# Performance work log

Measured on AMD Instinct MI355X. Metric: run time of the kernel, lower is better.

The kernel has to match this reference:

```python
import jax, jax.numpy as jnp
import numpy as np
import math

B, N, M, DK, H = 2, 2048, 2048, 512, 512  # input_v == hidden_size == H


def _lin(x, w, b):
    # torch Linear: y = x @ W.T + b, w: [out, in]
    return jnp.einsum('bnd,od->bno', x, w) + b


def setup_inputs() -> dict:
    key = jax.random.key(0)
    ks = jax.random.split(key, 20)
    s = 0.02
    d = {
        'KEY': jax.random.normal(ks[0], (B, N, DK), jnp.float32),
        'VALUE': jax.random.normal(ks[1], (B, N, H), jnp.float32),
        'QUERY': jax.random.normal(ks[2], (B, M, DK), jnp.float32),
        # W MLP: input_k -> hidden -> hidden -> input_k
        'W1_w': jax.random.normal(ks[3], (H, DK), jnp.float32) * s,
        'W1_b': jnp.zeros((H,), jnp.float32),
        'W2_w': jax.random.normal(ks[4], (H, H), jnp.float32) * s,
        'W2_b': jnp.zeros((H,), jnp.float32),
        'W3_w': jax.random.normal(ks[5], (DK, H), jnp.float32) * s,
        'W3_b': jnp.zeros((DK,), jnp.float32),
        # Wv MLP: input_v -> hidden -> hidden -> hidden
        'V1_w': jax.random.normal(ks[6], (H, H), jnp.float32) * s,
        'V1_b': jnp.zeros((H,), jnp.float32),
        'V2_w': jax.random.normal(ks[7], (H, H), jnp.float32) * s,
        'V2_b': jnp.zeros((H,), jnp.float32),
        'V3_w': jax.random.normal(ks[8], (H, H), jnp.float32) * s,
        'V3_b': jnp.zeros((H,), jnp.float32),
        # Wo: hidden -> input_v
        'Wo_w': jax.random.normal(ks[9], (H, H), jnp.float32) * s,
        'Wo_b': jnp.zeros((H,), jnp.float32),
    }
    return d


def reference(KEY, VALUE, QUERY, W1_w, W1_b, W2_w, W2_b, W3_w, W3_b,
              V1_w, V1_b, V2_w, V2_b, V3_w, V3_b, Wo_w, Wo_b):
    def mlp(x, w1, b1, w2, b2, w3, b3):
        h = jax.nn.relu(_lin(x, w1, b1))
        h = jax.nn.relu(_lin(h, w2, b2))
        return _lin(h, w3, b3)

    Wk = mlp(KEY, W1_w, W1_b, W2_w, W2_b, W3_w, W3_b)      # [b,n,dk]
    Wq = mlp(QUERY, W1_w, W1_b, W2_w, W2_b, W3_w, W3_b)    # [b,m,dk]
    Wv = mlp(VALUE, V1_w, V1_b, V2_w, V2_b, V3_w, V3_b)    # [b,n,h]

    KEY_s = KEY * Wk
    QUERY_s = QUERY * Wq
    VALUE_s = VALUE * Wv

    d_wk = KEY_s.shape[-1]
    dist = jnp.einsum('bij,bkj->bik', KEY_s, QUERY_s) / math.sqrt(d_wk)  # [b,n,m]
    weights = jax.nn.softmax(-(dist ** 2) * 0.5, axis=1)  # softmax over keys
    context = jnp.einsum('bik,bij->bkj', weights, VALUE_s)  # [b,m,h]
    # dropout is identity in eval mode
    return _lin(context, Wo_w, Wo_b)  # [b,m,input_v]
```

## Files before the change

### kernel.cpp

```cpp
#include <hip/hip_runtime.h>
#include <math.h>

typedef unsigned short u16;
typedef unsigned int u32;
typedef __attribute__((ext_vector_type(8))) short short8;
typedef __attribute__((ext_vector_type(4))) float f32x4;
typedef __attribute__((ext_vector_type(4))) u16 u16x4;

__device__ __forceinline__ void gload16(const void* g, void* l) {
    __builtin_amdgcn_global_load_lds(
        (__attribute__((address_space(1))) u32*)g,
        (__attribute__((address_space(3))) u32*)l, 16, 0, 0);
}

__device__ __forceinline__ u16 f2bf_rne(float v) {
    u32 u = __builtin_bit_cast(u32, v);
    return (u16)((u + 0x7FFFu + ((u >> 16) & 1u)) >> 16);
}
__device__ __forceinline__ float bf2f(u16 h) {
    u32 u = ((u32)h) << 16;
    return __builtin_bit_cast(float, u);
}
__device__ __forceinline__ void splt(float v, u16& h, u16& l) {
    h = f2bf_rne(v);
    l = f2bf_rne(v - bf2f(h));
}

enum { EP_RELU, EP_MUL };
enum { EP_DIST16, EP_PART };
enum { RM_CHUNK, RM_DIST2D };

template<int EP>
__global__ __launch_bounds__(256)
void mlp_pf(const u16* __restrict__ Ah, const u16* __restrict__ Al,
            const u16* __restrict__ BHkq, const u16* __restrict__ BLkq,
            const u16* __restrict__ BHv, const u16* __restrict__ BLv,
            const float* __restrict__ bias_kq, const float* __restrict__ bias_v,
            const float* __restrict__ Xk, const float* __restrict__ Xq,
            const float* __restrict__ Xv,
            u16* __restrict__ Ch, u16* __restrict__ Cl)
{
    __shared__ u16 LAh[2][128 * 32];
    __shared__ u16 LAl[2][128 * 32];
    __shared__ u16 LBh[2][64 * 32];
    __shared__ u16 LBl[2][64 * 32];

    const int tid = threadIdx.x;
    const int lane = tid & 63;
    const int wave = tid >> 6;
    const int wr = wave >> 1, wc = wave & 1;
    const int fr = lane & 15, kg = lane >> 4;

    const int L = blockIdx.y * 8 + blockIdx.x;
    const int xcd = L & 7;
    const int i = L >> 3;
    const int panel = xcd * 12 + (i >> 3);
    const int m0 = panel * 128, n0 = (i & 7) * 64;
    const int sec = panel >> 5;

    const u16* Bh = (sec == 2) ? BHv : BHkq;
    const u16* Bl = (sec == 2) ? BLv : BLkq;
    const float* bias = (sec == 2) ? bias_v : bias_kq;

    f32x4 acc[4][2];
    #pragma unroll
    for (int a = 0; a < 4; ++a)
        #pragma unroll
        for (int j = 0; j < 2; ++j)
            acc[a][j] = (f32x4){0.f, 0.f, 0.f, 0.f};

    auto STAGE = [&](int buf, int kk) {
        #pragma unroll
        for (int h = 0; h < 2; ++h) {
            int c = h * 256 + tid;
            long so = (long)(m0 + (c >> 2)) * 512 + kk + (c & 3) * 8;
            gload16(Ah + so, &LAh[buf][c * 8]);
        }
        #pragma unroll
        for (int h = 0; h < 2; ++h) {
            int c = h * 256 + tid;
            long so = (long)(m0 + (c >> 2)) * 512 + kk + (c & 3) * 8;
            gload16(Al + so, &LAl[buf][c * 8]);
        }
        {
            int c = tid;
            long so = (long)(n0 + (c >> 2)) * 512 + kk + (c & 3) * 8;
            gload16(Bh + so, &LBh[buf][c * 8]);
            gload16(Bl + so, &LBl[buf][c * 8]);
        }
    };

    auto COMPUTE = [&](int buf) {
        short8 ah[4], al[4], bh[2], bl[2];
        #pragma unroll
        for (int a = 0; a < 4; ++a) {
            int off = (wr * 64 + a * 16 + fr) * 32 + kg * 8;
            ah[a] = *(const short8*)&LAh[buf][off];
            al[a] = *(const short8*)&LAl[buf][off];
        }
        #pragma unroll
        for (int j = 0; j < 2; ++j) {
            int off = (wc * 32 + j * 16 + fr) * 32 + kg * 8;
            bh[j] = *(const short8*)&LBh[buf][off];
            bl[j] = *(const short8*)&LBl[buf][off];
        }
        #pragma unroll
        for (int a = 0; a < 4; ++a)
            #pragma unroll
            for (int j = 0; j < 2; ++j) {
                acc[a][j] = __builtin_amdgcn_mfma_f32_16x16x32_bf16(ah[a], bh[j], acc[a][j], 0, 0, 0);
                acc[a][j] = __builtin_amdgcn_mfma_f32_16x16x32_bf16(ah[a], bl[j], acc[a][j], 0, 0, 0);
                acc[a][j] = __builtin_amdgcn_mfma_f32_16x16x32_bf16(al[a], bh[j], acc[a][j], 0, 0, 0);
            }
    };

    STAGE(0, 0);
    int cur = 0;
    for (int t = 0; t < 15; ++t) {
        STAGE(cur ^ 1, (t + 1) << 5);
        asm volatile("s_waitcnt vmcnt(6)" ::: "memory");
        __builtin_amdgcn_s_barrier();
        COMPUTE(cur);
        __builtin_amdgcn_s_barrier();
        cur ^= 1;
    }
    asm volatile("s_waitcnt vmcnt(0)" ::: "memory");
    __builtin_amdgcn_s_barrier();
    COMPUTE(cur);

    const float* X = (EP == EP_MUL) ? ((sec == 0) ? Xk : (sec == 1) ? Xq : Xv) : nullptr;

    #pragma unroll
    for (int a = 0; a < 4; ++a)
        #pragma unroll
        for (int j = 0; j < 2; ++j)
            #pragma unroll
            for (int r = 0; r < 4; ++r) {
                int row = m0 + wr * 64 + a * 16 + kg * 4 + r;
                int col = n0 + wc * 32 + j * 16 + fr;
                float v = acc[a][j][r] + bias[col];
                if constexpr (EP == EP_RELU) {
                    v = fmaxf(v, 0.f);
                } else {
                    v *= X[(long)(row - (sec << 12)) * 512 + col];
                }
                long o = (long)row * 512 + col;
                u16 h, l; splt(v, h, l);
                Ch[o] = h; Cl[o] = l;
            }
}

template<int EP, int RM>
__global__ __launch_bounds__(256)
void gemm_pf(int K, int nsl, int KS,
             const u16* __restrict__ Ah, const u16* __restrict__ Al, int lda, long sA,
             const u16* __restrict__ Bh, const u16* __restrict__ Bl, int ldb, long sB,
             float* __restrict__ Cf, u16* __restrict__ Ch, u16* __restrict__ Cl,
             int ldc, long sC)
{
    __shared__ u16 LAh[2][128 * 32];
    __shared__ u16 LAl[2][128 * 32];
    __shared__ u16 LBh[2][64 * 32];
    __shared__ u16 LBl[2][64 * 32];

    const int tid = threadIdx.x;
    const int lane = tid & 63;
    const int wave = tid >> 6;
    const int wr = wave >> 1, wc = wave & 1;
    const int fr = lane & 15, kg = lane >> 4;

    int bx, by, bz;
    {
        const int gx = gridDim.x, gy = gridDim.y;
        const int L = (blockIdx.z * gy + blockIdx.y) * gx + blockIdx.x;
        const int xcd = L & 7;
        const int i = L >> 3;
        if constexpr (RM == RM_DIST2D) {
            const int c = i >> 6, pos = i & 63;
            const int chunk = c * 8 + xcd;
            const int mp = (chunk & 3) * 8 + (pos >> 3);
            bx = (chunk >> 2) * 8 + (pos & 7);
            by = mp & 15;
            bz = mp >> 4;
        } else {
            const int P = gy * gridDim.z;
            const int ppx = P >> 3;
            const int xt = i % gx;
            const int panel = xcd * ppx + i / gx;
            bx = xt;
            by = panel % gy;
            bz = panel / gy;
        }
    }

    const int b = bz / nsl;
    const int s = bz - b * nsl;
    const int k0 = s * KS;
    int k1 = k0 + KS; if (k1 > K) k1 = K;
    const int nt = (k1 - k0) >> 5;

    Ah += b * sA; Al += b * sA;
    Bh += b * sB; Bl += b * sB;
    const long cb = (long)bz * sC;

    const int m0 = by * 128, n0 = bx * 64;

    f32x4 acc[4][2];
    #pragma unroll
    for (int a = 0; a < 4; ++a)
        #pragma unroll
        for (int j = 0; j < 2; ++j)
            acc[a][j] = (f32x4){0.f, 0.f, 0.f, 0.f};

    auto STAGE = [&](int buf, int kk) {
        #pragma unroll
        for (int h = 0; h < 2; ++h) {
            int c = h * 256 + tid;
            long so = (long)(m0 + (c >> 2)) * lda + kk + (c & 3) * 8;
            gload16(Ah + so, &LAh[buf][c * 8]);
        }
        #pragma unroll
        for (int h = 0; h < 2; ++h) {
            int c = h * 256 + tid;
            long so = (long)(m0 + (c >> 2)) * lda + kk + (c & 3) * 8;
            gload16(Al + so, &LAl[buf][c * 8]);
        }
        {
            int c = tid;
            long so = (long)(n0 + (c >> 2)) * ldb + kk + (c & 3) * 8;
            gload16(Bh + so, &LBh[buf][c * 8]);
            gload16(Bl + so, &LBl[buf][c * 8]);
        }
    };

    auto COMPUTE = [&](int buf) {
        short8 ah[4], al[4], bh[2], bl[2];
        #pragma unroll
        for (int a = 0; a < 4; ++a) {
            int off = (wr * 64 + a * 16 + fr) * 32 + kg * 8;
            ah[a] = *(const short8*)&LAh[buf][off];
            al[a] = *(const short8*)&LAl[buf][off];
        }
        #pragma unroll
        for (int j = 0; j < 2; ++j) {
            int off = (wc * 32 + j * 16 + fr) * 32 + kg * 8;
            bh[j] = *(const short8*)&LBh[buf][off];
            bl[j] = *(const short8*)&LBl[buf][off];
        }
        #pragma unroll
        for (int a = 0; a < 4; ++a)
            #pragma unroll
            for (int j = 0; j < 2; ++j) {
                acc[a][j] = __builtin_amdgcn_mfma_f32_16x16x32_bf16(ah[a], bh[j], acc[a][j], 0, 0, 0);
                acc[a][j] = __builtin_amdgcn_mfma_f32_16x16x32_bf16(ah[a], bl[j], acc[a][j], 0, 0, 0);
                acc[a][j] = __builtin_amdgcn_mfma_f32_16x16x32_bf16(al[a], bh[j], acc[a][j], 0, 0, 0);
            }
    };

    STAGE(0, k0);
    int cur = 0;
    for (int t = 0; t < nt - 1; ++t) {
        STAGE(cur ^ 1, k0 + ((t + 1) << 5));
        asm volatile("s_waitcnt vmcnt(6)" ::: "memory");
        __builtin_amdgcn_s_barrier();
        COMPUTE(cur);
        __builtin_amdgcn_s_barrier();
        cur ^= 1;
    }
    asm volatile("s_waitcnt vmcnt(0)" ::: "memory");
    __builtin_amdgcn_s_barrier();
    COMPUTE(cur);

    #pragma unroll
    for (int a = 0; a < 4; ++a)
        #pragma unroll
        for (int j = 0; j < 2; ++j)
            #pragma unroll
            for (int r = 0; r < 4; ++r) {
                int row = m0 + wr * 64 + a * 16 + kg * 4 + r;
                int col = n0 + wc * 32 + j * 16 + fr;
                float v = acc[a][j][r];
                long o = cb + (long)row * ldc + col;
                if constexpr (EP == EP_DIST16) {
                    v = -(v * v) * (1.0f / 1024.0f);
                    u16 h, l; splt(v, h, l);
                    Ch[o] = h; Cl[o] = l;
                } else {
                    Cf[o] = v;
                }
            }
}

__global__ __launch_bounds__(256)
void softmax16(u16* __restrict__ S)
{
    long row = blockIdx.x;
    u16* hi = S + row * 4096;
    u16* lo = hi + 2048;
    int tid = threadIdx.x;
    int lane = tid & 63, w = tid >> 6;

    u16x4 h0 = ((u16x4*)hi)[tid * 2];
    u16x4 h1 = ((u16x4*)hi)[tid * 2 + 1];
    u16x4 l0 = ((u16x4*)lo)[tid * 2];
    u16x4 l1 = ((u16x4*)lo)[tid * 2 + 1];

    float v[8];
    #pragma unroll
    for (int i = 0; i < 4; ++i) {
        v[i]     = bf2f(h0[i]) + bf2f(l0[i]);
        v[4 + i] = bf2f(h1[i]) + bf2f(l1[i]);
    }

    float m = v[0];
    #pragma unroll
    for (int i = 1; i < 8; ++i) m = fmaxf(m, v[i]);
    #pragma unroll
    for (int o = 32; o; o >>= 1) m = fmaxf(m, __shfl_xor(m, o));

    __shared__ float redm[4];
    __shared__ float reds[4];
    if (lane == 0) redm[w] = m;
    __syncthreads();
    m = fmaxf(fmaxf(redm[0], redm[1]), fmaxf(redm[2], redm[3]));

    float s = 0.f;
    #pragma unroll
    for (int i = 0; i < 8; ++i) { v[i] = expf(v[i] - m); s += v[i]; }
    #pragma unroll
    for (int o = 32; o; o >>= 1) s += __shfl_xor(s, o);
    if (lane == 0) reds[w] = s;
    __syncthreads();
    s = reds[0] + reds[1] + reds[2] + reds[3];
    float inv = 1.0f / s;

    u16 h, l;
    #pragma unroll
    for (int i = 0; i < 4; ++i) {
        splt(v[i] * inv, h, l);     h0[i] = h; l0[i] = l;
        splt(v[4 + i] * inv, h, l); h1[i] = h; l1[i] = l;
    }
    ((u16x4*)hi)[tid * 2] = h0;
    ((u16x4*)hi)[tid * 2 + 1] = h1;
    ((u16x4*)lo)[tid * 2] = l0;
    ((u16x4*)lo)[tid * 2 + 1] = l1;
}

__global__ __launch_bounds__(256)
void transpose16(const u16* __restrict__ vH, const u16* __restrict__ vL,
                 u16* __restrict__ tH, u16* __restrict__ tL)
{
    __shared__ float t[32][33];
    int b = blockIdx.z;
    int c0 = blockIdx.x * 32;
    int r0 = blockIdx.y * 32;
    int tx = threadIdx.x, ty = threadIdx.y;
    #pragma unroll
    for (int k = 0; k < 4; ++k) {
        long idx = (long)(b * 2048 + r0 + ty + 8 * k) * 512 + c0 + tx;
        t[ty + 8 * k][tx] = bf2f(vH[idx]) + bf2f(vL[idx]);
    }
    __syncthreads();
    long ob = (long)b * 512 * 2048;
    #pragma unroll
    for (int k = 0; k < 4; ++k) {
        float v = t[tx][ty + 8 * k];
        u16 h, l; splt(v, h, l);
        long o = ob + (long)(c0 + ty + 8 * k) * 2048 + r0 + tx;
        tH[o] = h; tL[o] = l;
    }
}

__global__ __launch_bounds__(256)
void split_w(const float* __restrict__ w0, const float* __restrict__ w1,
             const float* __restrict__ w2, const float* __restrict__ w3,
             const float* __restrict__ w4, const float* __restrict__ w5,
             const float* __restrict__ w6, u16* __restrict__ dst)
{
    int wi = blockIdx.y;
    const float* src;
    switch (wi) {
        case 0: src = w0; break; case 1: src = w1; break;
        case 2: src = w2; break; case 3: src = w3; break;
        case 4: src = w4; break; case 5: src = w5; break;
        default: src = w6; break;
    }
    u16* hi = dst + (long)wi * 524288;
    u16* lo = hi + 262144;
    int i = blockIdx.x * 256 + threadIdx.x;
    float4 v = ((const float4*)src)[i];
    u16x4 h4, l4; u16 h, l;
    splt(v.x, h, l); h4.x = h; l4.x = l;
    splt(v.y, h, l); h4.y = h; l4.y = l;
    splt(v.z, h, l); h4.z = h; l4.z = l;
    splt(v.w, h, l); h4.w = h; l4.w = l;
    ((u16x4*)hi)[i] = h4;
    ((u16x4*)lo)[i] = l4;
}

__global__ __launch_bounds__(256)
void split_in(const float* __restrict__ k, const float* __restrict__ q,
              const float* __restrict__ vv, u16* __restrict__ hi, u16* __restrict__ lo)
{
    int sec = blockIdx.y;
    const float* src = (sec == 0) ? k : (sec == 1) ? q : vv;
    long base4 = (long)sec * 524288;
    int i = blockIdx.x * 256 + threadIdx.x;
    float4 v = ((const float4*)src)[i];
    u16x4 h4, l4; u16 h, l;
    splt(v.x, h, l); h4.x = h; l4.x = l;
    splt(v.y, h, l); h4.y = h; l4.y = l;
    splt(v.z, h, l); h4.z = h; l4.z = l;
    splt(v.w, h, l); h4.w = h; l4.w = l;
    ((u16x4*)(hi))[base4 + i] = h4;
    ((u16x4*)(lo))[base4 + i] = l4;
}

__global__ __launch_bounds__(256)
void reduce_ctx(const float* __restrict__ P, u16* __restrict__ ctH, u16* __restrict__ ctL)
{
    int i4 = blockIdx.x * 256 + threadIdx.x;
    long e = (long)i4 * 4;
    int b = (int)(e >> 20);
    long r = e & ((1L << 20) - 1);
    const float* base = P + ((long)(b * 3) << 20) + r;
    float4 v0 = *(const float4*)base;
    float4 v1 = *(const float4*)(base + (1L << 20));
    float4 v2 = *(const float4*)(base + (2L << 20));
    u16x4 h4, l4; u16 h, l;
    splt(v0.x + v1.x + v2.x, h, l); h4.x = h; l4.x = l;
    splt(v0.y + v1.y + v2.y, h, l); h4.y = h; l4.y = l;
    splt(v0.z + v1.z + v2.z, h, l); h4.z = h; l4.z = l;
    splt(v0.w + v1.w + v2.w, h, l); h4.w = h; l4.w = l;
    ((u16x4*)ctH)[i4] = h4;
    ((u16x4*)ctL)[i4] = l4;
}

__global__ __launch_bounds__(256)
void reduce_out(const float* __restrict__ P, const float* __restrict__ bias,
                float* __restrict__ out)
{
    int i4 = blockIdx.x * 256 + threadIdx.x;
    long e = (long)i4 * 4;
    float4 a = ((const float4*)P)[i4];
    float4 c = ((const float4*)(P + 2097152))[i4];
    float4 bb = *(const float4*)(bias + (e & 511));
    float4 o;
    o.x = a.x + c.x + bb.x;
    o.y = a.y + c.y + bb.y;
    o.z = a.z + c.z + bb.z;
    o.w = a.w + c.w + bb.w;
    ((float4*)out)[i4] = o;
}

extern "C" void kernel_launch(void* const* d_in, const int* in_sizes, int n_in,
                              void* d_out, int out_size, void* d_ws, size_t ws_size,
                              hipStream_t stream)
{
    const float* KEY   = (const float*)d_in[0];
    const float* VALUE = (const float*)d_in[1];
    const float* QUERY = (const float*)d_in[2];
    const float* W1w = (const float*)d_in[3];
    const float* W1b = (const float*)d_in[4];
    const float* W2w = (const float*)d_in[5];
    const float* W2b = (const float*)d_in[6];
    const float* W3w = (const float*)d_in[7];
    const float* W3b = (const float*)d_in[8];
    const float* V1w = (const float*)d_in[9];
    const float* V1b = (const float*)d_in[10];
    const float* V2w = (const float*)d_in[11];
    const float* V2b = (const float*)d_in[12];
    const float* V3w = (const float*)d_in[13];
    const float* V3b = (const float*)d_in[14];
    const float* Wow = (const float*)d_in[15];
    const float* Wob = (const float*)d_in[16];
    float* out = (float*)d_out;

    const long SEC  = 4096L * 512;
    const long FULL = 3 * SEC;

    u16* Wb = (u16*)d_ws;
    u16* cH = Wb + 3670016;
    u16* cL = cH + FULL;
    u16* R1 = cL + FULL;
    u16* h1H = R1,            *h1L = R1 + FULL;
    u16* h2H = R1 + 2 * FULL, *h2L = R1 + 3 * FULL;
    u16* sTu = R1;
    u16* vtH = R1 + 16777216;
    u16* vtL = vtH + 2097152;
    u16* ctH = R1 + 20971520;
    u16* ctL = ctH + 2097152;
    float* Pctx = (float*)cH;
    float* Pout = (float*)cH;

    u16* wH6 = Wb + 6L * 524288;
    u16* wL6 = wH6 + 262144;

    dim3 blk(256);

    split_w<<<dim3(256, 7), blk, 0, stream>>>(W1w, W2w, W3w, V1w, V2w, V3w, Wow, Wb);
    split_in<<<dim3(2048, 3), blk, 0, stream>>>(KEY, QUERY, VALUE, cH, cL);

    dim3 gL(8, 96, 1);
    mlp_pf<EP_RELU><<<gL, blk, 0, stream>>>(
        cH, cL, Wb, Wb + 262144, Wb + 3 * 524288, Wb + 3 * 524288 + 262144,
        W1b, V1b, nullptr, nullptr, nullptr, h1H, h1L);
    mlp_pf<EP_RELU><<<gL, blk, 0, stream>>>(
        h1H, h1L, Wb + 524288, Wb + 524288 + 262144, Wb + 4 * 524288, Wb + 4 * 524288 + 262144,
        W2b, V2b, nullptr, nullptr, nullptr, h2H, h2L);
    mlp_pf<EP_MUL><<<gL, blk, 0, stream>>>(
        h2H, h2L, Wb + 2 * 524288, Wb + 2 * 524288 + 262144, Wb + 5 * 524288, Wb + 5 * 524288 + 262144,
        W3b, V3b, KEY, QUERY, VALUE, cH, cL);

    transpose16<<<dim3(16, 64, 2), dim3(32, 8), 0, stream>>>(
        cH + 2 * SEC, cL + 2 * SEC, vtH, vtL);

    gemm_pf<EP_DIST16, RM_DIST2D><<<dim3(32, 16, 2), blk, 0, stream>>>(
        512, 1, 512,
        cH + SEC, cL + SEC, 512, 1048576,
        cH, cL, 512, 1048576,
        nullptr, sTu, sTu + 2048, 4096, 8388608);

    softmax16<<<dim3(4096), blk, 0, stream>>>(sTu);

    gemm_pf<EP_PART, RM_CHUNK><<<dim3(8, 16, 6), blk, 0, stream>>>(
        2048, 3, 704,
        sTu, sTu + 2048, 4096, 8388608,
        vtH, vtL, 2048, 1048576,
        Pctx, nullptr, nullptr, 512, 1048576);

    reduce_ctx<<<dim3(2048), blk, 0, stream>>>(Pctx, ctH, ctL);

    gemm_pf<EP_PART, RM_CHUNK><<<dim3(8, 32, 2), blk, 0, stream>>>(
        512, 2, 256,
        ctH, ctL, 512, 0,
        wH6, wL6, 512, 0,
        Pout, nullptr, nullptr, 512, 2097152);

    reduce_out<<<dim3(2048), blk, 0, stream>>>(Pout, Wob, out);
}
```

Baseline: 221.4 us.

## Fuse V transpose into MLP epilogue, enlarge tiles to 128x128, rebalance split-K

```diff
diff --git a/kernel.cpp b/kernel.cpp
--- a/kernel.cpp
+++ b/kernel.cpp
@@ -27,23 +27,23 @@
 }
 
 enum { EP_RELU, EP_MUL };
-enum { EP_DIST16, EP_PART };
-enum { RM_CHUNK, RM_DIST2D };
+enum { EP_PART };
 
 template<int EP>
 __global__ __launch_bounds__(256)
-void mlp_pf(const u16* __restrict__ Ah, const u16* __restrict__ Al,
-            const u16* __restrict__ BHkq, const u16* __restrict__ BLkq,
-            const u16* __restrict__ BHv, const u16* __restrict__ BLv,
-            const float* __restrict__ bias_kq, const float* __restrict__ bias_v,
-            const float* __restrict__ Xk, const float* __restrict__ Xq,
-            const float* __restrict__ Xv,
-            u16* __restrict__ Ch, u16* __restrict__ Cl)
+void mlp2(const u16* __restrict__ Ah, const u16* __restrict__ Al,
+          const u16* __restrict__ BHkq, const u16* __restrict__ BLkq,
+          const u16* __restrict__ BHv, const u16* __restrict__ BLv,
+          const float* __restrict__ bias_kq, const float* __restrict__ bias_v,
+          const float* __restrict__ Xk, const float* __restrict__ Xq,
+          const float* __restrict__ Xv,
+          u16* __restrict__ Ch, u16* __restrict__ Cl,
+          u16* __restrict__ vtH, u16* __restrict__ vtL)
 {
     __shared__ u16 LAh[2][128 * 32];
     __shared__ u16 LAl[2][128 * 32];
-    __shared__ u16 LBh[2][64 * 32];
-    __shared__ u16 LBl[2][64 * 32];
+    __shared__ u16 LBh[2][128 * 32];
+    __shared__ u16 LBl[2][128 * 32];
 
     const int tid = threadIdx.x;
     const int lane = tid & 63;
@@ -51,22 +51,22 @@
     const int wr = wave >> 1, wc = wave & 1;
     const int fr = lane & 15, kg = lane >> 4;
 
-    const int L = blockIdx.y * 8 + blockIdx.x;
+    const int L = blockIdx.y * 4 + blockIdx.x;
     const int xcd = L & 7;
     const int i = L >> 3;
-    const int panel = xcd * 12 + (i >> 3);
-    const int m0 = panel * 128, n0 = (i & 7) * 64;
+    const int panel = xcd * 12 + (i >> 2);
+    const int m0 = panel * 128, n0 = (i & 3) * 128;
     const int sec = panel >> 5;
 
     const u16* Bh = (sec == 2) ? BHv : BHkq;
     const u16* Bl = (sec == 2) ? BLv : BLkq;
     const float* bias = (sec == 2) ? bias_v : bias_kq;
 
-    f32x4 acc[4][2];
+    f32x4 acc[4][4];
     #pragma unroll
     for (int a = 0; a < 4; ++a)
         #pragma unroll
-        for (int j = 0; j < 2; ++j)
+        for (int j = 0; j < 4; ++j)
             acc[a][j] = (f32x4){0.f, 0.f, 0.f, 0.f};
 
     auto STAGE = [&](int buf, int kk) {
@@ -82,16 +82,22 @@
             long so = (long)(m0 + (c >> 2)) * 512 + kk + (c & 3) * 8;
             gload16(Al + so, &LAl[buf][c * 8]);
         }
-        {
-            int c = tid;
+        #pragma unroll
+        for (int h = 0; h < 2; ++h) {
+            int c = h * 256 + tid;
             long so = (long)(n0 + (c >> 2)) * 512 + kk + (c & 3) * 8;
             gload16(Bh + so, &LBh[buf][c * 8]);
+        }
+        #pragma unroll
+        for (int h = 0; h < 2; ++h) {
+            int c = h * 256 + tid;
+            long so = (long)(n0 + (c >> 2)) * 512 + kk + (c & 3) * 8;
             gload16(Bl + so, &LBl[buf][c * 8]);
         }
     };
 
     auto COMPUTE = [&](int buf) {
-        short8 ah[4], al[4], bh[2], bl[2];
+        short8 ah[4], al[4], bh[4], bl[4];
         #pragma unroll
         for (int a = 0; a < 4; ++a) {
             int off = (wr * 64 + a * 16 + fr) * 32 + kg * 8;
@@ -99,15 +105,15 @@
             al[a] = *(const short8*)&LAl[buf][off];
         }
         #pragma unroll
-        for (int j = 0; j < 2; ++j) {
-            int off = (wc * 32 + j * 16 + fr) * 32 + kg * 8;
+        for (int j = 0; j < 4; ++j) {
+            int off = (wc * 64 + j * 16 + fr) * 32 + kg * 8;
             bh[j] = *(const short8*)&LBh[buf][off];
             bl[j] = *(const short8*)&LBl[buf][off];
         }
         #pragma unroll
         for (int a = 0; a < 4; ++a)
             #pragma unroll
-            for (int j = 0; j < 2; ++j) {
+            for (int j = 0; j < 4; ++j) {
                 acc[a][j] = __builtin_amdgcn_mfma_f32_16x16x32_bf16(ah[a], bh[j], acc[a][j], 0, 0, 0);
                 acc[a][j] = __builtin_amdgcn_mfma_f32_16x16x32_bf16(ah[a], bl[j], acc[a][j], 0, 0, 0);
                 acc[a][j] = __builtin_amdgcn_mfma_f32_16x16x32_bf16(al[a], bh[j], acc[a][j], 0, 0, 0);
@@ -118,7 +124,7 @@
     int cur = 0;
     for (int t = 0; t < 15; ++t) {
         STAGE(cur ^ 1, (t + 1) << 5);
-        asm volatile("s_waitcnt vmcnt(6)" ::: "memory");
+        asm volatile("s_waitcnt vmcnt(8)" ::: "memory");
         __builtin_amdgcn_s_barrier();
         COMPUTE(cur);
         __builtin_amdgcn_s_barrier();
@@ -133,30 +139,157 @@
     #pragma unroll
     for (int a = 0; a < 4; ++a)
         #pragma unroll
-        for (int j = 0; j < 2; ++j)
+        for (int j = 0; j < 4; ++j)
             #pragma unroll
             for (int r = 0; r < 4; ++r) {
                 int row = m0 + wr * 64 + a * 16 + kg * 4 + r;
-                int col = n0 + wc * 32 + j * 16 + fr;
+                int col = n0 + wc * 64 + j * 16 + fr;
                 float v = acc[a][j][r] + bias[col];
+                u16 h, l;
                 if constexpr (EP == EP_RELU) {
                     v = fmaxf(v, 0.f);
+                    splt(v, h, l);
+                    long o = (long)row * 512 + col;
+                    Ch[o] = h; Cl[o] = l;
                 } else {
                     v *= X[(long)(row - (sec << 12)) * 512 + col];
+                    splt(v, h, l);
+                    if (sec < 2) {
+                        long o = (long)row * 512 + col;
+                        Ch[o] = h; Cl[o] = l;
+                    } else {
+                        int rb = row - 8192;
+                        long o = (long)(rb >> 11) * 1048576 + (long)col * 2048 + (rb & 2047);
+                        vtH[o] = h; vtL[o] = l;
+                    }
                 }
-                long o = (long)row * 512 + col;
+            }
+}
+
+__global__ __launch_bounds__(256)
+void dist2(const u16* __restrict__ QH, const u16* __restrict__ QL,
+           const u16* __restrict__ KH, const u16* __restrict__ KL,
+           u16* __restrict__ S)
+{
+    __shared__ u16 LAh[2][128 * 32];
+    __shared__ u16 LAl[2][128 * 32];
+    __shared__ u16 LBh[2][128 * 32];
+    __shared__ u16 LBl[2][128 * 32];
+
+    const int tid = threadIdx.x;
+    const int lane = tid & 63;
+    const int wave = tid >> 6;
+    const int wr = wave >> 1, wc = wave & 1;
+    const int fr = lane & 15, kg = lane >> 4;
+
+    const int L = (blockIdx.z * 16 + blockIdx.y) * 16 + blockIdx.x;
+    const int xcd = L & 7;
+    const int pos = L >> 3;
+    const int b = xcd >> 2, quad = xcd & 3;
+    const int mi = (quad >> 1) * 8 + (pos >> 3);
+    const int ni = (quad & 1) * 8 + (pos & 7);
+    const int m0 = mi * 128, n0 = ni * 128;
+
+    const u16* Ah = QH + (long)b * 1048576;
+    const u16* Al = QL + (long)b * 1048576;
+    const u16* Bh = KH + (long)b * 1048576;
+    const u16* Bl = KL + (long)b * 1048576;
+
+    f32x4 acc[4][4];
+    #pragma unroll
+    for (int a = 0; a < 4; ++a)
+        #pragma unroll
+        for (int j = 0; j < 4; ++j)
+            acc[a][j] = (f32x4){0.f, 0.f, 0.f, 0.f};
+
+    auto STAGE = [&](int buf, int kk) {
+        #pragma unroll
+        for (int h = 0; h < 2; ++h) {
+            int c = h * 256 + tid;
+            long so = (long)(m0 + (c >> 2)) * 512 + kk + (c & 3) * 8;
+            gload16(Ah + so, &LAh[buf][c * 8]);
+        }
+        #pragma unroll
+        for (int h = 0; h < 2; ++h) {
+            int c = h * 256 + tid;
+            long so = (long)(m0 + (c >> 2)) * 512 + kk + (c & 3) * 8;
+            gload16(Al + so, &LAl[buf][c * 8]);
+        }
+        #pragma unroll
+        for (int h = 0; h < 2; ++h) {
+            int c = h * 256 + tid;
+            long so = (long)(n0 + (c >> 2)) * 512 + kk + (c & 3) * 8;
+            gload16(Bh + so, &LBh[buf][c * 8]);
+        }
+        #pragma unroll
+        for (int h = 0; h < 2; ++h) {
+            int c = h * 256 + tid;
+            long so = (long)(n0 + (c >> 2)) * 512 + kk + (c & 3) * 8;
+            gload16(Bl + so, &LBl[buf][c * 8]);
+        }
+    };
+
+    auto COMPUTE = [&](int buf) {
+        short8 ah[4], al[4], bh[4], bl[4];
+        #pragma unroll
+        for (int a = 0; a < 4; ++a) {
+            int off = (wr * 64 + a * 16 + fr) * 32 + kg * 8;
+            ah[a] = *(const short8*)&LAh[buf][off];
+            al[a] = *(const short8*)&LAl[buf][off];
+        }
+        #pragma unroll
+        for (int j = 0; j < 4; ++j) {
+            int off = (wc * 64 + j * 16 + fr) * 32 + kg * 8;
+            bh[j] = *(const short8*)&LBh[buf][off];
+            bl[j] = *(const short8*)&LBl[buf][off];
+        }
+        #pragma unroll
+        for (int a = 0; a < 4; ++a)
+            #pragma unroll
+            for (int j = 0; j < 4; ++j) {
+                acc[a][j] = __builtin_amdgcn_mfma_f32_16x16x32_bf16(ah[a], bh[j], acc[a][j], 0, 0, 0);
+                acc[a][j] = __builtin_amdgcn_mfma_f32_16x16x32_bf16(ah[a], bl[j], acc[a][j], 0, 0, 0);
+                acc[a][j] = __builtin_amdgcn_mfma_f32_16x16x32_bf16(al[a], bh[j], acc[a][j], 0, 0, 0);
+            }
+    };
+
+    STAGE(0, 0);
+    int cur = 0;
+    for (int t = 0; t < 15; ++t) {
+        STAGE(cur ^ 1, (t + 1) << 5);
+        asm volatile("s_waitcnt vmcnt(8)" ::: "memory");
+        __builtin_amdgcn_s_barrier();
+        COMPUTE(cur);
+        __builtin_amdgcn_s_barrier();
+        cur ^= 1;
+    }
+    asm volatile("s_waitcnt vmcnt(0)" ::: "memory");
+    __builtin_amdgcn_s_barrier();
+    COMPUTE(cur);
+
+    u16* Sb = S + (long)b * 8388608;
+    #pragma unroll
+    for (int a = 0; a < 4; ++a)
+        #pragma unroll
+        for (int j = 0; j < 4; ++j)
+            #pragma unroll
+            for (int r = 0; r < 4; ++r) {
+                int row = m0 + wr * 64 + a * 16 + kg * 4 + r;
+                int col = n0 + wc * 64 + j * 16 + fr;
+                float v = acc[a][j][r];
+                v = -(v * v) * (1.0f / 1024.0f);
                 u16 h, l; splt(v, h, l);
-                Ch[o] = h; Cl[o] = l;
+                u16* p = Sb + (long)row * 4096 + col;
+                p[0] = h; p[2048] = l;
             }
 }
 
-template<int EP, int RM>
+template<int EP>
 __global__ __launch_bounds__(256)
 void gemm_pf(int K, int nsl, int KS,
              const u16* __restrict__ Ah, const u16* __restrict__ Al, int lda, long sA,
              const u16* __restrict__ Bh, const u16* __restrict__ Bl, int ldb, long sB,
-             float* __restrict__ Cf, u16* __restrict__ Ch, u16* __restrict__ Cl,
-             int ldc, long sC)
+             float* __restrict__ Cf, int ldc, long sC)
 {
     __shared__ u16 LAh[2][128 * 32];
     __shared__ u16 LAl[2][128 * 32];
@@ -175,22 +308,12 @@
         const int L = (blockIdx.z * gy + blockIdx.y) * gx + blockIdx.x;
         const int xcd = L & 7;
         const int i = L >> 3;
-        if constexpr (RM == RM_DIST2D) {
-            const int c = i >> 6, pos = i & 63;
-            const int chunk = c * 8 + xcd;
-            const int mp = (chunk & 3) * 8 + (pos >> 3);
-            bx = (chunk >> 2) * 8 + (pos & 7);
-            by = mp & 15;
-            bz = mp >> 4;
-        } else {
-            const int P = gy * gridDim.z;
-            const int ppx = P >> 3;
-            const int xt = i % gx;
-            const int panel = xcd * ppx + i / gx;
-            bx = xt;
-            by = panel % gy;
-            bz = panel / gy;
-        }
+        const int P = gy * gridDim.z;
+        const int ppx = P >> 3;
+        bx = i % gx;
+        const int panel = xcd * ppx + i / gx;
+        by = panel % gy;
+        bz = panel / gy;
     }
 
     const int b = bz / nsl;
@@ -279,15 +402,7 @@
             for (int r = 0; r < 4; ++r) {
                 int row = m0 + wr * 64 + a * 16 + kg * 4 + r;
                 int col = n0 + wc * 32 + j * 16 + fr;
-                float v = acc[a][j][r];
-                long o = cb + (long)row * ldc + col;
-                if constexpr (EP == EP_DIST16) {
-                    v = -(v * v) * (1.0f / 1024.0f);
-                    u16 h, l; splt(v, h, l);
-                    Ch[o] = h; Cl[o] = l;
-                } else {
-                    Cf[o] = v;
-                }
+                Cf[cb + (long)row * ldc + col] = acc[a][j][r];
             }
 }
 
@@ -344,31 +459,6 @@
     ((u16x4*)hi)[tid * 2 + 1] = h1;
     ((u16x4*)lo)[tid * 2] = l0;
     ((u16x4*)lo)[tid * 2 + 1] = l1;
-}
-
-__global__ __launch_bounds__(256)
-void transpose16(const u16* __restrict__ vH, const u16* __restrict__ vL,
-                 u16* __restrict__ tH, u16* __restrict__ tL)
-{
-    __shared__ float t[32][33];
-    int b = blockIdx.z;
-    int c0 = blockIdx.x * 32;
-    int r0 = blockIdx.y * 32;
-    int tx = threadIdx.x, ty = threadIdx.y;
-    #pragma unroll
-    for (int k = 0; k < 4; ++k) {
-        long idx = (long)(b * 2048 + r0 + ty + 8 * k) * 512 + c0 + tx;
-        t[ty + 8 * k][tx] = bf2f(vH[idx]) + bf2f(vL[idx]);
-    }
-    __syncthreads();
-    long ob = (long)b * 512 * 2048;
-    #pragma unroll
-    for (int k = 0; k < 4; ++k) {
-        float v = t[tx][ty + 8 * k];
-        u16 h, l; splt(v, h, l);
-        long o = ob + (long)(c0 + ty + 8 * k) * 2048 + r0 + tx;
-        tH[o] = h; tL[o] = l;
-    }
 }
 
 __global__ __launch_bounds__(256)
@@ -423,15 +513,14 @@
     long e = (long)i4 * 4;
     int b = (int)(e >> 20);
     long r = e & ((1L << 20) - 1);
-    const float* base = P + ((long)(b * 3) << 20) + r;
+    const float* base = P + ((long)(b * 2) << 20) + r;
     float4 v0 = *(const float4*)base;
     float4 v1 = *(const float4*)(base + (1L << 20));
-    float4 v2 = *(const float4*)(base + (2L << 20));
     u16x4 h4, l4; u16 h, l;
-    splt(v0.x + v1.x + v2.x, h, l); h4.x = h; l4.x = l;
-    splt(v0.y + v1.y + v2.y, h, l); h4.y = h; l4.y = l;
-    splt(v0.z + v1.z + v2.z, h, l); h4.z = h; l4.z = l;
-    splt(v0.w + v1.w + v2.w, h, l); h4.w = h; l4.w = l;
+    splt(v0.x + v1.x, h, l); h4.x = h; l4.x = l;
+    splt(v0.y + v1.y, h, l); h4.y = h; l4.y = l;
+    splt(v0.z + v1.z, h, l); h4.z = h; l4.z = l;
+    splt(v0.w + v1.w, h, l); h4.w = h; l4.w = l;
     ((u16x4*)ctH)[i4] = h4;
     ((u16x4*)ctL)[i4] = l4;
 }
@@ -476,22 +565,21 @@
     const float* Wob = (const float*)d_in[16];
     float* out = (float*)d_out;
 
-    const long SEC  = 4096L * 512;
+    const long SEC  = 2097152;
     const long FULL = 3 * SEC;
 
     u16* Wb = (u16*)d_ws;
-    u16* cH = Wb + 3670016;
-    u16* cL = cH + FULL;
-    u16* R1 = cL + FULL;
-    u16* h1H = R1,            *h1L = R1 + FULL;
-    u16* h2H = R1 + 2 * FULL, *h2L = R1 + 3 * FULL;
-    u16* sTu = R1;
-    u16* vtH = R1 + 16777216;
-    u16* vtL = vtH + 2097152;
-    u16* ctH = R1 + 20971520;
-    u16* ctL = ctH + 2097152;
-    float* Pctx = (float*)cH;
-    float* Pout = (float*)cH;
+    u16* B0p = Wb + 3670016;
+    u16* cH = B0p;            u16* cL = B0p + FULL;
+    u16* h1H = B0p + 6 * SEC; u16* h1L = B0p + 9 * SEC;
+    u16* h2H = B0p + 12 * SEC; u16* h2L = B0p + 15 * SEC;
+    u16* ksH = B0p;            u16* ksL = B0p + FULL;
+    u16* qsH = B0p + SEC;
+    u16* vtH = B0p + 2 * SEC;  u16* vtL = B0p + FULL + 2 * SEC;
+    u16* sTu = B0p + 6 * SEC;
+    float* Pctx = (float*)(B0p + 14 * SEC);
+    u16* ctH = B0p;            u16* ctL = B0p + SEC;
+    float* Pout = (float*)(B0p + 14 * SEC);
 
     u16* wH6 = Wb + 6L * 524288;
     u16* wL6 = wH6 + 262144;
@@ -501,41 +589,34 @@
     split_w<<<dim3(256, 7), blk, 0, stream>>>(W1w, W2w, W3w, V1w, V2w, V3w, Wow, Wb);
     split_in<<<dim3(2048, 3), blk, 0, stream>>>(KEY, QUERY, VALUE, cH, cL);
 
-    dim3 gL(8, 96, 1);
-    mlp_pf<EP_RELU><<<gL, blk, 0, stream>>>(
+    dim3 gL(4, 96, 1);
+    mlp2<EP_RELU><<<gL, blk, 0, stream>>>(
         cH, cL, Wb, Wb + 262144, Wb + 3 * 524288, Wb + 3 * 524288 + 262144,
-        W1b, V1b, nullptr, nullptr, nullptr, h1H, h1L);
-    mlp_pf<EP_RELU><<<gL, blk, 0, stream>>>(
+        W1b, V1b, nullptr, nullptr, nullptr, h1H, h1L, nullptr, nullptr);
+    mlp2<EP_RELU><<<gL, blk, 0, stream>>>(
         h1H, h1L, Wb + 524288, Wb + 524288 + 262144, Wb + 4 * 524288, Wb + 4 * 524288 + 262144,
-        W2b, V2b, nullptr, nullptr, nullptr, h2H, h2L);
-    mlp_pf<EP_MUL><<<gL, blk, 0, stream>>>(
+        W2b, V2b, nullptr, nullptr, nullptr, h2H, h2L, nullptr, nullptr);
+    mlp2<EP_MUL><<<gL, blk, 0, stream>>>(
         h2H, h2L, Wb + 2 * 524288, Wb + 2 * 524288 + 262144, Wb + 5 * 524288, Wb + 5 * 524288 + 262144,
-        W3b, V3b, KEY, QUERY, VALUE, cH, cL);
-
-    transpose16<<<dim3(16, 64, 2), dim3(32, 8), 0, stream>>>(
-        cH + 2 * SEC, cL + 2 * SEC, vtH, vtL);
-
-    gemm_pf<EP_DIST16, RM_DIST2D><<<dim3(32, 16, 2), blk, 0, stream>>>(
-        512, 1, 512,
-        cH + SEC, cL + SEC, 512, 1048576,
-        cH, cL, 512, 1048576,
-        nullptr, sTu, sTu + 2048, 4096, 8388608);
+        W3b, V3b, KEY, QUERY, VALUE, ksH, ksL, vtH, vtL);
+
+    dist2<<<dim3(16, 16, 2), blk, 0, stream>>>(qsH, qsH + FULL, ksH, ksL, sTu);
 
     softmax16<<<dim3(4096), blk, 0, stream>>>(sTu);
 
-    gemm_pf<EP_PART, RM_CHUNK><<<dim3(8, 16, 6), blk, 0, stream>>>(
-        2048, 3, 704,
+    gemm_pf<EP_PART><<<dim3(8, 16, 4), blk, 0, stream>>>(
+        2048, 2, 1024,
         sTu, sTu + 2048, 4096, 8388608,
         vtH, vtL, 2048, 1048576,
-        Pctx, nullptr, nullptr, 512, 1048576);
+        Pctx, 512, 1048576);
 
     reduce_ctx<<<dim3(2048), blk, 0, stream>>>(Pctx, ctH, ctL);
 
-    gemm_pf<EP_PART, RM_CHUNK><<<dim3(8, 32, 2), blk, 0, stream>>>(
+    gemm_pf<EP_PART><<<dim3(8, 32, 2), blk, 0, stream>>>(
         512, 2, 256,
         ctH, ctL, 512, 0,
         wH6, wL6, 512, 0,
-        Pout, nullptr, nullptr, 512, 2097152);
+        Pout, 512, 2097152);
 
     reduce_out<<<dim3(2048), blk, 0, stream>>>(Pout, Wob, out);
 }
```

New measurement: 235.7 us. 6.5% more time.
